# Kernel optimization log

Measured on AMD Instinct MI355X. Metric: run time of the kernel, lower is better.

Reference implementation:

```python
import jax, jax.numpy as jnp
import numpy as np

BOND_TOL = 0.4
CLASH_TOL = 1.5
IDEAL_CA_CA = 3.8
EPS = 1e-08


def setup_inputs() -> dict:
    key = jax.random.key(0)
    k1, _ = jax.random.split(key)
    B, L = 8, 2048
    positions = jax.random.normal(k1, (B, L, 3), dtype=jnp.float32) * 10.0
    mask = jnp.ones((B, L), dtype=jnp.float32)
    return {"positions": positions, "mask": mask}


def reference(positions, mask):
    # positions: [B, L, 3] CA coordinates; mask: [B, L]
    L = positions.shape[1]
    ca = positions
    ca_mask = mask

    # --- bond term: consecutive CA-CA distances ---
    ca_diff = ca[:, 1:] - ca[:, :-1]                       # [B, L-1, 3]
    ca_dist = jnp.sqrt(jnp.sum(ca_diff ** 2, axis=-1) + EPS)
    bond_violation = jax.nn.relu(jnp.abs(ca_dist - IDEAL_CA_CA) - BOND_TOL)
    bond_mask = ca_mask[:, 1:] * ca_mask[:, :-1]
    bond_loss = jnp.sum(bond_violation * bond_mask) / (jnp.sum(bond_mask) + EPS)

    # --- clash term: all-pairs distances, non-bonded (|i-j| > 2) ---
    all_diff = ca[:, :, None, :] - ca[:, None, :, :]       # [B, L, L, 3]
    all_dist = jnp.sqrt(jnp.sum(all_diff ** 2, axis=-1) + EPS)  # [B, L, L]
    idx = jnp.arange(L)
    seq_sep = jnp.abs(idx[None, :] - idx[:, None])         # [L, L]
    non_bonded = (seq_sep > 2).astype(ca.dtype)
    clash_violation = jax.nn.relu(CLASH_TOL - all_dist)
    pair_mask = ca_mask[:, :, None] * ca_mask[:, None, :] * non_bonded[None]
    clash_loss = jnp.sum(clash_violation * pair_mask) / (jnp.sum(pair_mask) + EPS)

    total = bond_loss + clash_loss
    # stacked: [bond_loss, clash_loss, total_violation]
    return jnp.stack([bond_loss, clash_loss, total])
```

## Files before the change

### kernel.cpp

```cpp
#include <hip/hip_runtime.h>

#define TPB 256
#define RPB 8
#define SEQ_L 2048
#define CHUNK 256
#define NCH (SEQ_L / CHUNK)
#define NBATCH 8
#define NPAIR 128
#define NBLOCKS (NBATCH * NPAIR)
#define NWAVE (TPB / 64)

static constexpr float kBondTol  = 0.4f;
static constexpr float kClashTol = 1.5f;
static constexpr float kIdeal    = 3.8f;
static constexpr float kEps      = 1e-8f;
static constexpr float kThresh2  = 2.25f;
static constexpr float kFarBase  = 1.0e5f;
static constexpr float kHugeD2   = 1.0e12f;

__device__ __forceinline__ float wred(float v) {
#pragma unroll
  for (int o = 32; o > 0; o >>= 1) v += __shfl_down(v, o, 64);
  return v;
}

__global__ __launch_bounds__(TPB, 4) void viol_main(
    const float* __restrict__ pos,
    const float* __restrict__ mask,
    float4* __restrict__ partial) {
  __shared__ float sx[SEQ_L], sy[SEQ_L], sz[SEQ_L];
  __shared__ float redm[NWAVE];
  __shared__ float red4[NWAVE][4];

  const int b   = blockIdx.x & 7;
  const int t   = blockIdx.x >> 3;
  const int i0A = t << 3;
  const int i0B = (255 - t) << 3;
  const int k0A = i0A >> 8;
  const int k0B = i0B >> 8;

  const float* pb = pos  + (size_t)b * SEQ_L * 3;
  const float* mb = mask + (size_t)b * SEQ_L;

  float mpart = 0.f;
#pragma unroll
  for (int it = 0; it < NCH; ++it) {
    const int idx = (int)threadIdx.x + (it << 8);
    const float m = mb[idx];
    mpart += m;
    if (it >= k0A) {
      float x = pb[3 * idx + 0];
      float y = pb[3 * idx + 1];
      float z = pb[3 * idx + 2];
      if (m == 0.f) { x = kFarBase + 4.f * (float)idx; y = 0.f; z = 0.f; }
      sx[idx] = x; sy[idx] = y; sz[idx] = z;
    }
  }
  mpart = wred(mpart);
  const int wid  = threadIdx.x >> 6;
  const int lane = threadIdx.x & 63;
  if (lane == 0) redm[wid] = mpart;
  __syncthreads();
  const float msum = redm[0] + redm[1] + redm[2] + redm[3];

  float pxA[RPB], pyA[RPB], pzA[RPB], accA[RPB];
  float pxB[RPB], pyB[RPB], pzB[RPB], accB[RPB];
#pragma unroll
  for (int q = 0; q < RPB; ++q) {
    pxA[q] = sx[i0A + q]; pyA[q] = sy[i0A + q]; pzA[q] = sz[i0A + q];
    pxB[q] = sx[i0B + q]; pyB[q] = sy[i0B + q]; pzB[q] = sz[i0B + q];
    accA[q] = 0.f; accB[q] = 0.f;
  }

  {
    int jc = (int)threadIdx.x + (k0A << 8);
    float cx = sx[jc], cy = sy[jc], cz = sz[jc];
    for (int k = k0A; k < NCH; ++k) {
      const int kn = (k + 1 < NCH) ? k + 1 : k;
      const int jn = (int)threadIdx.x + (kn << 8);
      const float nx = sx[jn], ny = sy[jn], nz = sz[jn];
      const int j = (int)threadIdx.x + (k << 8);

      float d2r[RPB];
#pragma unroll
      for (int q = 0; q < RPB; ++q) {
        const float dx = cx - pxA[q], dy = cy - pyA[q], dz = cz - pzA[q];
        d2r[q] = fmaf(dx, dx, fmaf(dy, dy, dz * dz));
      }
      if (k == k0A) {
#pragma unroll
        for (int q = 0; q < RPB; ++q)
          d2r[q] = (j > i0A + q) ? d2r[q] : kHugeD2;
      }
      {
        float mv = d2r[0];
#pragma unroll
        for (int q = 1; q < RPB; ++q) mv = fminf(mv, d2r[q]);
        if (__ballot(mv < kThresh2) != 0ull) {
#pragma unroll
          for (int q = 0; q < RPB; ++q) {
            const float dist = __builtin_amdgcn_sqrtf(d2r[q] + kEps);
            accA[q] += fmaxf(kClashTol - dist, 0.f);
          }
        }
      }
      if (k >= k0B) {
#pragma unroll
        for (int q = 0; q < RPB; ++q) {
          const float dx = cx - pxB[q], dy = cy - pyB[q], dz = cz - pzB[q];
          d2r[q] = fmaf(dx, dx, fmaf(dy, dy, dz * dz));
        }
        if (k == k0B) {
#pragma unroll
          for (int q = 0; q < RPB; ++q)
            d2r[q] = (j > i0B + q) ? d2r[q] : kHugeD2;
        }
        float mv = d2r[0];
#pragma unroll
        for (int q = 1; q < RPB; ++q) mv = fminf(mv, d2r[q]);
        if (__ballot(mv < kThresh2) != 0ull) {
#pragma unroll
          for (int q = 0; q < RPB; ++q) {
            const float dist = __builtin_amdgcn_sqrtf(d2r[q] + kEps);
            accB[q] += fmaxf(kClashTol - dist, 0.f);
          }
        }
      }
      cx = nx; cy = ny; cz = nz;
    }
  }

  float cv = 0.f;
#pragma unroll
  for (int q = 0; q < RPB; ++q) cv += accA[q] + accB[q];

  float bv = 0.f, bm = 0.f, pm = 0.f;
  if (threadIdx.x < 16) {
    const int i = ((threadIdx.x & 8) ? i0B : i0A) + (int)(threadIdx.x & 7);
    const float xi = sx[i], yi = sy[i], zi = sz[i];
    const int jhi = (i + 2 > SEQ_L - 1) ? SEQ_L - 1 : i + 2;
    float nv = 0.f;
    for (int j = i + 1; j <= jhi; ++j) {
      const float dx = sx[j] - xi, dy = sy[j] - yi, dz = sz[j] - zi;
      const float dist = __builtin_amdgcn_sqrtf(dx*dx + dy*dy + dz*dz + kEps);
      nv += fmaxf(kClashTol - dist, 0.f);
    }
    cv -= nv;

    const float mi = mb[i];
    float nm = 0.f;
    const int jlo = (i - 2 < 0) ? 0 : i - 2;
    for (int j = jlo; j <= jhi; ++j) nm += mb[j];
    pm = mi * (msum - nm);

    if (i < SEQ_L - 1) {
      const float dx = sx[i+1] - xi, dy = sy[i+1] - yi, dz = sz[i+1] - zi;
      const float dist = __builtin_amdgcn_sqrtf(dx*dx + dy*dy + dz*dz + kEps);
      const float mj = mb[i + 1];
      bv = fmaxf(fabsf(dist - kIdeal) - kBondTol, 0.f) * mi * mj;
      bm = mi * mj;
    }
  }

  bv = wred(bv); bm = wred(bm); cv = wred(cv); pm = wred(pm);
  if (lane == 0) {
    red4[wid][0] = bv; red4[wid][1] = bm;
    red4[wid][2] = cv; red4[wid][3] = pm;
  }
  __syncthreads();
  if (threadIdx.x == 0) {
    float tbv = 0.f, tbm = 0.f, tcv = 0.f, tpm = 0.f;
#pragma unroll
    for (int w = 0; w < NWAVE; ++w) {
      tbv += red4[w][0]; tbm += red4[w][1];
      tcv += red4[w][2]; tpm += red4[w][3];
    }
    partial[blockIdx.x] = make_float4(tbv, tbm, 2.f * tcv, tpm);
  }
}

__global__ __launch_bounds__(TPB) void viol_reduce(
    const float4* __restrict__ partial, float* __restrict__ out) {
  __shared__ float red4[NWAVE][4];
  float bv = 0.f, bm = 0.f, cv = 0.f, pm = 0.f;
#pragma unroll
  for (int i = threadIdx.x; i < NBLOCKS; i += TPB) {
    float4 p = partial[i];
    bv += p.x; bm += p.y; cv += p.z; pm += p.w;
  }
  bv = wred(bv); bm = wred(bm); cv = wred(cv); pm = wred(pm);
  const int wid  = threadIdx.x >> 6;
  const int lane = threadIdx.x & 63;
  if (lane == 0) {
    red4[wid][0] = bv; red4[wid][1] = bm;
    red4[wid][2] = cv; red4[wid][3] = pm;
  }
  __syncthreads();
  if (threadIdx.x == 0) {
    float tbv = 0.f, tbm = 0.f, tcv = 0.f, tpm = 0.f;
#pragma unroll
    for (int w = 0; w < NWAVE; ++w) {
      tbv += red4[w][0]; tbm += red4[w][1];
      tcv += red4[w][2]; tpm += red4[w][3];
    }
    float bond  = tbv / (tbm + kEps);
    float clash = tcv / (tpm + kEps);
    out[0] = bond;
    out[1] = clash;
    out[2] = bond + clash;
  }
}

extern "C" void kernel_launch(void* const* d_in, const int* in_sizes, int n_in,
                              void* d_out, int out_size, void* d_ws, size_t ws_size,
                              hipStream_t stream) {
  const float* pos  = (const float*)d_in[0];
  const float* mask = (const float*)d_in[1];
  float* out = (float*)d_out;
  float4* partial = (float4*)d_ws;

  viol_main<<<dim3(NBLOCKS), dim3(TPB), 0, stream>>>(pos, mask, partial);
  viol_reduce<<<dim3(1), dim3(TPB), 0, stream>>>(partial, out);
}
```

Measured before the change: 64.02 us.

## Fuse final reduction via atomic counter and drop LDS staging with smaller row tiles

Replaces the two-kernel main+reduce scheme with one kernel where the last block to finish, detected via an atomic counter, reduces all partials. Drops shared-memory staging of coordinates in favour of direct global loads, halves rows per block while doubling block count, and raises occupancy hints. Mask sum is computed only by t==0 blocks and added as msum squared. This adds a memset launch and relies on cached global loads instead of LDS.

```diff
diff --git a/kernel.cpp b/kernel.cpp
--- a/kernel.cpp
+++ b/kernel.cpp
@@ -1,12 +1,12 @@
 #include <hip/hip_runtime.h>
 
 #define TPB 256
-#define RPB 8
+#define RPB 4
 #define SEQ_L 2048
-#define CHUNK 256
-#define NCH (SEQ_L / CHUNK)
+#define NCH 8
 #define NBATCH 8
-#define NPAIR 128
+#define NT4 512
+#define NPAIR 256
 #define NBLOCKS (NBATCH * NPAIR)
 #define NWAVE (TPB / 64)
 
@@ -24,62 +24,65 @@
   return v;
 }
 
-__global__ __launch_bounds__(TPB, 4) void viol_main(
+__global__ __launch_bounds__(TPB, 8) void viol_fused(
     const float* __restrict__ pos,
     const float* __restrict__ mask,
-    float4* __restrict__ partial) {
-  __shared__ float sx[SEQ_L], sy[SEQ_L], sz[SEQ_L];
+    float4* __restrict__ partial,
+    unsigned* __restrict__ counter,
+    float* __restrict__ out) {
+  __shared__ float red4[NWAVE][4];
   __shared__ float redm[NWAVE];
-  __shared__ float red4[NWAVE][4];
 
   const int b   = blockIdx.x & 7;
   const int t   = blockIdx.x >> 3;
-  const int i0A = t << 3;
-  const int i0B = (255 - t) << 3;
-  const int k0A = i0A >> 8;
-  const int k0B = i0B >> 8;
+  const int i0A = t << 2;
+  const int i0B = (NT4 - 1 - t) << 2;
+  const int k0A = t >> 6;
+  const int k0B = (NT4 - 1 - t) >> 6;
+  const int tid  = (int)threadIdx.x;
+  const int wid  = tid >> 6;
+  const int lane = tid & 63;
 
   const float* pb = pos  + (size_t)b * SEQ_L * 3;
   const float* mb = mask + (size_t)b * SEQ_L;
 
-  float mpart = 0.f;
-#pragma unroll
-  for (int it = 0; it < NCH; ++it) {
-    const int idx = (int)threadIdx.x + (it << 8);
-    const float m = mb[idx];
-    mpart += m;
-    if (it >= k0A) {
-      float x = pb[3 * idx + 0];
-      float y = pb[3 * idx + 1];
-      float z = pb[3 * idx + 2];
-      if (m == 0.f) { x = kFarBase + 4.f * (float)idx; y = 0.f; z = 0.f; }
-      sx[idx] = x; sy[idx] = y; sz[idx] = z;
-    }
-  }
-  mpart = wred(mpart);
-  const int wid  = threadIdx.x >> 6;
-  const int lane = threadIdx.x & 63;
-  if (lane == 0) redm[wid] = mpart;
-  __syncthreads();
-  const float msum = redm[0] + redm[1] + redm[2] + redm[3];
+  float msq = 0.f;
+  if (t == 0) {
+    float mp = 0.f;
+#pragma unroll
+    for (int it = 0; it < NCH; ++it) mp += mb[tid + (it << 8)];
+    mp = wred(mp);
+    if (lane == 0) redm[wid] = mp;
+    __syncthreads();
+    const float ms = redm[0] + redm[1] + redm[2] + redm[3];
+    msq = ms * ms;
+  }
 
   float pxA[RPB], pyA[RPB], pzA[RPB], accA[RPB];
   float pxB[RPB], pyB[RPB], pzB[RPB], accB[RPB];
 #pragma unroll
   for (int q = 0; q < RPB; ++q) {
-    pxA[q] = sx[i0A + q]; pyA[q] = sy[i0A + q]; pzA[q] = sz[i0A + q];
-    pxB[q] = sx[i0B + q]; pyB[q] = sy[i0B + q]; pzB[q] = sz[i0B + q];
+    const int iA = i0A + q, iB = i0B + q;
+    float xA = pb[3 * iA], yA = pb[3 * iA + 1], zA = pb[3 * iA + 2];
+    float xB = pb[3 * iB], yB = pb[3 * iB + 1], zB = pb[3 * iB + 2];
+    if (mb[iA] == 0.f) { xA = kFarBase + 4.f * (float)iA; yA = 0.f; zA = 0.f; }
+    if (mb[iB] == 0.f) { xB = kFarBase + 4.f * (float)iB; yB = 0.f; zB = 0.f; }
+    pxA[q] = xA; pyA[q] = yA; pzA[q] = zA;
+    pxB[q] = xB; pyB[q] = yB; pzB[q] = zB;
     accA[q] = 0.f; accB[q] = 0.f;
   }
 
   {
-    int jc = (int)threadIdx.x + (k0A << 8);
-    float cx = sx[jc], cy = sy[jc], cz = sz[jc];
+    int jg = tid + (k0A << 8);
+    float cx = pb[3 * jg], cy = pb[3 * jg + 1], cz = pb[3 * jg + 2];
+    if (mb[jg] == 0.f) { cx = kFarBase + 4.f * (float)jg; cy = 0.f; cz = 0.f; }
+
     for (int k = k0A; k < NCH; ++k) {
       const int kn = (k + 1 < NCH) ? k + 1 : k;
-      const int jn = (int)threadIdx.x + (kn << 8);
-      const float nx = sx[jn], ny = sy[jn], nz = sz[jn];
-      const int j = (int)threadIdx.x + (k << 8);
+      const int jn = tid + (kn << 8);
+      float nx = pb[3 * jn], ny = pb[3 * jn + 1], nz = pb[3 * jn + 2];
+      const float nm = mb[jn];
+      const int j = tid + (k << 8);
 
       float d2r[RPB];
 #pragma unroll
@@ -93,9 +96,7 @@
           d2r[q] = (j > i0A + q) ? d2r[q] : kHugeD2;
       }
       {
-        float mv = d2r[0];
-#pragma unroll
-        for (int q = 1; q < RPB; ++q) mv = fminf(mv, d2r[q]);
+        const float mv = fminf(fminf(d2r[0], d2r[1]), fminf(d2r[2], d2r[3]));
         if (__ballot(mv < kThresh2) != 0ull) {
 #pragma unroll
           for (int q = 0; q < RPB; ++q) {
@@ -115,9 +116,7 @@
           for (int q = 0; q < RPB; ++q)
             d2r[q] = (j > i0B + q) ? d2r[q] : kHugeD2;
         }
-        float mv = d2r[0];
-#pragma unroll
-        for (int q = 1; q < RPB; ++q) mv = fminf(mv, d2r[q]);
+        const float mv = fminf(fminf(d2r[0], d2r[1]), fminf(d2r[2], d2r[3]));
         if (__ballot(mv < kThresh2) != 0ull) {
 #pragma unroll
           for (int q = 0; q < RPB; ++q) {
@@ -126,6 +125,7 @@
           }
         }
       }
+      if (nm == 0.f) { nx = kFarBase + 4.f * (float)jn; ny = 0.f; nz = 0.f; }
       cx = nx; cy = ny; cz = nz;
     }
   }
@@ -135,26 +135,33 @@
   for (int q = 0; q < RPB; ++q) cv += accA[q] + accB[q];
 
   float bv = 0.f, bm = 0.f, pm = 0.f;
-  if (threadIdx.x < 16) {
-    const int i = ((threadIdx.x & 8) ? i0B : i0A) + (int)(threadIdx.x & 7);
-    const float xi = sx[i], yi = sy[i], zi = sz[i];
+  if (tid < 8) {
+    const int i = (tid < 4) ? (i0A + tid) : (i0B + (tid - 4));
+    const float mi = mb[i];
+    const float xi = pb[3 * i], yi = pb[3 * i + 1], zi = pb[3 * i + 2];
+    float sxi = xi, syi = yi, szi = zi;
+    if (mi == 0.f) { sxi = kFarBase + 4.f * (float)i; syi = 0.f; szi = 0.f; }
     const int jhi = (i + 2 > SEQ_L - 1) ? SEQ_L - 1 : i + 2;
+
     float nv = 0.f;
-    for (int j = i + 1; j <= jhi; ++j) {
-      const float dx = sx[j] - xi, dy = sy[j] - yi, dz = sz[j] - zi;
+    for (int jj = i + 1; jj <= jhi; ++jj) {
+      float xj = pb[3 * jj], yj = pb[3 * jj + 1], zj = pb[3 * jj + 2];
+      if (mb[jj] == 0.f) { xj = kFarBase + 4.f * (float)jj; yj = 0.f; zj = 0.f; }
+      const float dx = xj - sxi, dy = yj - syi, dz = zj - szi;
       const float dist = __builtin_amdgcn_sqrtf(dx*dx + dy*dy + dz*dz + kEps);
       nv += fmaxf(kClashTol - dist, 0.f);
     }
     cv -= nv;
 
-    const float mi = mb[i];
-    float nm = 0.f;
+    float nm_ = 0.f;
     const int jlo = (i - 2 < 0) ? 0 : i - 2;
-    for (int j = jlo; j <= jhi; ++j) nm += mb[j];
-    pm = mi * (msum - nm);
+    for (int jj = jlo; jj <= jhi; ++jj) nm_ += mb[jj];
+    pm = -mi * nm_;
 
     if (i < SEQ_L - 1) {
-      const float dx = sx[i+1] - xi, dy = sy[i+1] - yi, dz = sz[i+1] - zi;
+      const float dx = pb[3*(i+1)]   - xi;
+      const float dy = pb[3*(i+1)+1] - yi;
+      const float dz = pb[3*(i+1)+2] - zi;
       const float dist = __builtin_amdgcn_sqrtf(dx*dx + dy*dy + dz*dz + kEps);
       const float mj = mb[i + 1];
       bv = fmaxf(fabsf(dist - kIdeal) - kBondTol, 0.f) * mi * mj;
@@ -168,46 +175,49 @@
     red4[wid][2] = cv; red4[wid][3] = pm;
   }
   __syncthreads();
-  if (threadIdx.x == 0) {
+
+  int lastflag = 0;
+  if (tid == 0) {
     float tbv = 0.f, tbm = 0.f, tcv = 0.f, tpm = 0.f;
 #pragma unroll
     for (int w = 0; w < NWAVE; ++w) {
       tbv += red4[w][0]; tbm += red4[w][1];
       tcv += red4[w][2]; tpm += red4[w][3];
     }
-    partial[blockIdx.x] = make_float4(tbv, tbm, 2.f * tcv, tpm);
-  }
-}
-
-__global__ __launch_bounds__(TPB) void viol_reduce(
-    const float4* __restrict__ partial, float* __restrict__ out) {
-  __shared__ float red4[NWAVE][4];
-  float bv = 0.f, bm = 0.f, cv = 0.f, pm = 0.f;
-#pragma unroll
-  for (int i = threadIdx.x; i < NBLOCKS; i += TPB) {
-    float4 p = partial[i];
-    bv += p.x; bm += p.y; cv += p.z; pm += p.w;
-  }
-  bv = wred(bv); bm = wred(bm); cv = wred(cv); pm = wred(pm);
-  const int wid  = threadIdx.x >> 6;
-  const int lane = threadIdx.x & 63;
-  if (lane == 0) {
-    red4[wid][0] = bv; red4[wid][1] = bm;
-    red4[wid][2] = cv; red4[wid][3] = pm;
-  }
-  __syncthreads();
-  if (threadIdx.x == 0) {
-    float tbv = 0.f, tbm = 0.f, tcv = 0.f, tpm = 0.f;
-#pragma unroll
-    for (int w = 0; w < NWAVE; ++w) {
-      tbv += red4[w][0]; tbm += red4[w][1];
-      tcv += red4[w][2]; tpm += red4[w][3];
-    }
-    float bond  = tbv / (tbm + kEps);
-    float clash = tcv / (tpm + kEps);
-    out[0] = bond;
-    out[1] = clash;
-    out[2] = bond + clash;
+    tpm += msq;
+    float* p = (float*)(partial + blockIdx.x);
+    __hip_atomic_store(p + 0, tbv,       __ATOMIC_RELAXED, __HIP_MEMORY_SCOPE_AGENT);
+    __hip_atomic_store(p + 1, tbm,       __ATOMIC_RELAXED, __HIP_MEMORY_SCOPE_AGENT);
+    __hip_atomic_store(p + 2, 2.f * tcv, __ATOMIC_RELAXED, __HIP_MEMORY_SCOPE_AGENT);
+    __hip_atomic_store(p + 3, tpm,       __ATOMIC_RELAXED, __HIP_MEMORY_SCOPE_AGENT);
+    asm volatile("s_waitcnt vmcnt(0)" ::: "memory");
+    lastflag = ((unsigned)atomicAdd(counter, 1u) == NBLOCKS - 1u) ? 1 : 0;
+  }
+
+  if (wid == 0) {
+    lastflag = __shfl(lastflag, 0, 64);
+    if (lastflag) {
+      float rbv = 0.f, rbm = 0.f, rcv = 0.f, rpm = 0.f;
+      for (int idx = lane; idx < NBLOCKS; idx += 64) {
+        const unsigned long long* q = (const unsigned long long*)(partial + idx);
+        const unsigned long long lo =
+            __hip_atomic_load(q + 0, __ATOMIC_RELAXED, __HIP_MEMORY_SCOPE_AGENT);
+        const unsigned long long hi =
+            __hip_atomic_load(q + 1, __ATOMIC_RELAXED, __HIP_MEMORY_SCOPE_AGENT);
+        rbv += __uint_as_float((unsigned)(lo & 0xffffffffull));
+        rbm += __uint_as_float((unsigned)(lo >> 32));
+        rcv += __uint_as_float((unsigned)(hi & 0xffffffffull));
+        rpm += __uint_as_float((unsigned)(hi >> 32));
+      }
+      rbv = wred(rbv); rbm = wred(rbm); rcv = wred(rcv); rpm = wred(rpm);
+      if (lane == 0) {
+        const float bond  = rbv / (rbm + kEps);
+        const float clash = rcv / (rpm + kEps);
+        out[0] = bond;
+        out[1] = clash;
+        out[2] = bond + clash;
+      }
+    }
   }
 }
 
@@ -217,8 +227,10 @@
   const float* pos  = (const float*)d_in[0];
   const float* mask = (const float*)d_in[1];
   float* out = (float*)d_out;
-  float4* partial = (float4*)d_ws;
-
-  viol_main<<<dim3(NBLOCKS), dim3(TPB), 0, stream>>>(pos, mask, partial);
-  viol_reduce<<<dim3(1), dim3(TPB), 0, stream>>>(partial, out);
+  float4* partial   = (float4*)d_ws;
+  unsigned* counter = (unsigned*)((char*)d_ws + NBLOCKS * sizeof(float4));
+
+  hipMemsetAsync(counter, 0, sizeof(unsigned), stream);
+  viol_fused<<<dim3(NBLOCKS), dim3(TPB), 0, stream>>>(pos, mask, partial,
+                                                      counter, out);
 }
```

Result: slower. 91.66 us (+43.2%).
